# Optimization experiments

Hardware: AMD Instinct MI355X
Metric: run time of the kernel (lower is better)

Reference implementation:

```python
import jax, jax.numpy as jnp
import numpy as np
import math

B, LA, LB, D, H = 8, 2048, 2048, 512, 512

def setup_inputs() -> dict:
    key = jax.random.key(0)
    ks = jax.random.split(key, 6)
    return {
        "input_a": jax.random.normal(ks[0], (B, LA, D), dtype=jnp.float32),
        "input_b": jax.random.normal(ks[1], (B, LB, D), dtype=jnp.float32),
        "mask_a": jax.random.randint(ks[2], (B, LA), 0, 2, dtype=jnp.int32),
        "mask_b": jax.random.randint(ks[3], (B, LB), 0, 2, dtype=jnp.int32),
        "Wa": jax.random.normal(ks[4], (D, H), dtype=jnp.float32) * (1.0 / math.sqrt(D)),
        "ba": jnp.zeros((H,), dtype=jnp.float32),
        "Wb": jax.random.normal(ks[5], (D, H), dtype=jnp.float32) * (1.0 / math.sqrt(D)),
        "bb": jnp.zeros((H,), dtype=jnp.float32),
    }

def reference(input_a, input_b, mask_a, mask_b, Wa, ba, Wb, bb):
    scale = 1.0 / math.sqrt(D)  # math.sqrt(input_dim_a)
    mapped_a = input_a @ Wa + ba            # [B, La, H]
    mapped_b = input_b @ Wb + bb            # [B, Lb, H]
    # final_mask = (mask_a outer mask_b) == 0
    final_mask = (mask_a[:, :, None] * mask_b[:, None, :]) == 0  # [B, La, Lb]
    scores = jnp.einsum('bih,bjh->bij', mapped_a, mapped_b) * scale
    scores = jnp.where(final_mask, jnp.float32(-1e9), scores)
    # attentions_a = softmax over Lb; attentions_b^T = softmax over La axis
    att_a = jax.nn.softmax(scores, axis=-1)   # [B, La, Lb]
    att_bT = jax.nn.softmax(scores, axis=1)   # [B, La, Lb] (= attentions_b.transpose(1,2))
    output_a = jnp.einsum('bij,bjd->bid', att_bT, input_b)  # [B, La, D]
    output_b = jnp.einsum('bij,bid->bjd', att_a, input_a)   # [B, Lb, D]
    return (output_a + input_a, output_b + input_b)
```

## Files before the change

kernel.cpp:

```cpp
#include <hip/hip_runtime.h>
#include <hip/hip_bf16.h>

#define BATCH 8
#define LSEQ 2048
#define DDIM 512

using f32x4 = __attribute__((ext_vector_type(4))) float;
using s16x8 = __attribute__((ext_vector_type(8))) short;
using s16x4 = __attribute__((ext_vector_type(4))) short;

static __device__ __forceinline__ unsigned short f2b(float f) {
  __hip_bfloat16 h = __float2bfloat16(f);
  return __builtin_bit_cast(unsigned short, h);
}
static __device__ __forceinline__ float b2f(unsigned short u) {
  unsigned int v = ((unsigned int)u) << 16;
  return __builtin_bit_cast(float, v);
}

static __device__ __forceinline__ void gld16(const unsigned short* g, unsigned short* l) {
  __builtin_amdgcn_global_load_lds(
      (__attribute__((address_space(1))) void*)(g),
      (__attribute__((address_space(3))) void*)(l), 16, 0, 0);
}

__device__ __forceinline__ void mfma_kloop2(
    const unsigned short* __restrict__ A, const unsigned short* __restrict__ Bt,
    int K, int lda, int ldb, unsigned short* sA, unsigned short* sB,
    int tid, f32x4 acc[4][4]) {
  const int wave = tid >> 6, lane = tid & 63;
  const int wm = (wave >> 1) * 64, wn = (wave & 1) * 64;
  const int lr = lane & 15, lq = lane >> 4;
  const int srow = tid >> 2;
  const int sk = (tid & 3) * 8;
  unsigned short* dA0 = sA + wave * 512;
  unsigned short* dA1 = sA + 2048 + wave * 512;
  unsigned short* dB0 = sB + wave * 512;
  unsigned short* dB1 = sB + 2048 + wave * 512;
  const unsigned short* pa0 = A + (size_t)srow * lda + sk;
  const unsigned short* pa1 = A + (size_t)(srow + 64) * lda + sk;
  const unsigned short* pb0 = Bt + (size_t)srow * ldb + sk;
  const unsigned short* pb1 = Bt + (size_t)(srow + 64) * ldb + sk;
  gld16(pa0, dA0);
  gld16(pa1, dA1);
  gld16(pb0, dB0);
  gld16(pb1, dB1);
  asm volatile("s_waitcnt vmcnt(0)\ns_barrier" ::: "memory");
  int cur = 0;
  for (int k0 = 0; k0 < K; k0 += 32) {
    const int nxt = cur ^ 1;
    if (k0 + 32 < K) {
      const int off = nxt * 4096;
      gld16(pa0 + k0 + 32, dA0 + off);
      gld16(pa1 + k0 + 32, dA1 + off);
      gld16(pb0 + k0 + 32, dB0 + off);
      gld16(pb1 + k0 + 32, dB1 + off);
    }
    const unsigned short* cA = sA + cur * 4096;
    const unsigned short* cB = sB + cur * 4096;
    s16x8 af[4], bf[4];
#pragma unroll
    for (int r = 0; r < 4; ++r)
      af[r] = *(const s16x8*)(cA + (wm + r * 16 + lr) * 32 + lq * 8);
#pragma unroll
    for (int c = 0; c < 4; ++c)
      bf[c] = *(const s16x8*)(cB + (wn + c * 16 + lr) * 32 + lq * 8);
#pragma unroll
    for (int r = 0; r < 4; ++r)
#pragma unroll
      for (int c = 0; c < 4; ++c)
        acc[r][c] = __builtin_amdgcn_mfma_f32_16x16x32_bf16(af[r], bf[c], acc[r][c], 0, 0, 0);
    asm volatile("s_waitcnt vmcnt(0)\ns_barrier" ::: "memory");
    cur = nxt;
  }
}

__global__ __launch_bounds__(256) void k_prep(const float* __restrict__ in_a,
                                              const float* __restrict__ in_b,
                                              const int* __restrict__ ma,
                                              const int* __restrict__ mb,
                                              unsigned short* __restrict__ oa,
                                              unsigned short* __restrict__ ob,
                                              float* __restrict__ Pa,
                                              float* __restrict__ Pb) {
  int z = blockIdx.z;
  const float* in = z ? in_b : in_a;
  const int* mask = z ? mb : ma;
  unsigned short* o16 = z ? ob : oa;
  float* partial = z ? Pb : Pa;
  int b = blockIdx.y;
  int l0 = blockIdx.x * 32;
  __shared__ int sm[32];
  if (threadIdx.x < 32) sm[threadIdx.x] = mask[b * LSEQ + l0 + threadIdx.x];
  __syncthreads();
  int d = threadIdx.x * 2;
  const float* base = in + ((size_t)b * LSEQ + l0) * DDIM + d;
  unsigned short* obase = o16 + ((size_t)b * LSEQ + l0) * DDIM + d;
  float ax = 0.f, ay = 0.f;
#pragma unroll 4
  for (int r = 0; r < 32; ++r) {
    float2 v = *(const float2*)(base + (size_t)r * DDIM);
    ushort2 u; u.x = f2b(v.x); u.y = f2b(v.y);
    *(ushort2*)(obase + (size_t)r * DDIM) = u;
    if (sm[r] == 0) { ax += v.x; ay += v.y; }
  }
  float2 o; o.x = ax; o.y = ay;
  *(float2*)(partial + ((size_t)(b * 64 + blockIdx.x)) * DDIM + d) = o;
}

__global__ __launch_bounds__(256) void k_p2(const float* __restrict__ Pa,
                                            const float* __restrict__ Pb,
                                            float* __restrict__ Ca,
                                            float* __restrict__ Cb) {
  int g = blockIdx.x;
  const float* src = (g < 8) ? Pa : Pb;
  float* dst = (g < 8) ? Ca : Cb;
  int b = g & 7;
  int d = threadIdx.x * 2;
  float ax = 0.f, ay = 0.f;
  for (int c = 0; c < 64; ++c) {
    float2 v = *(const float2*)(src + ((size_t)(b * 64 + c)) * DDIM + d);
    ax += v.x; ay += v.y;
  }
  dst[b * DDIM + d] = ax * (1.0f / LSEQ);
  dst[b * DDIM + d + 1] = ay * (1.0f / LSEQ);
}

__global__ __launch_bounds__(256) void k_transposeW(const float* __restrict__ Wa,
                                                    const float* __restrict__ Wb,
                                                    unsigned short* __restrict__ WaT,
                                                    unsigned short* __restrict__ WbT) {
  int gidx = blockIdx.x * 256 + threadIdx.x;
  const float* W = (gidx < 512 * 512) ? Wa : Wb;
  unsigned short* WT = (gidx < 512 * 512) ? WaT : WbT;
  int idx = gidx & (512 * 512 - 1);
  int h = idx >> 9, d = idx & 511;
  WT[idx] = f2b(W[d * DDIM + h]);
}

__global__ __launch_bounds__(256) void k_gemm_bias(const unsigned short* __restrict__ a16,
                                                   const unsigned short* __restrict__ b16,
                                                   const unsigned short* __restrict__ WaT,
                                                   const unsigned short* __restrict__ WbT,
                                                   const float* __restrict__ ba,
                                                   const float* __restrict__ bb,
                                                   unsigned short* __restrict__ mapa,
                                                   unsigned short* __restrict__ mapb) {
  int id = blockIdx.x;
  int g = id >> 5, rem = id & 31;
  int bn = (rem >> 3) * 128;
  int f = g * 8 + (rem & 7);
  int bm = (f & 127) * 128;
  int z = f >> 7;
  const unsigned short* A = z ? b16 : a16;
  const unsigned short* Bt = z ? WbT : WaT;
  const float* bias = z ? bb : ba;
  unsigned short* Cout = z ? mapb : mapa;
  __shared__ __align__(16) unsigned short sA[2 * 128 * 32], sB[2 * 128 * 32];
  f32x4 acc[4][4];
  f32x4 zero = {0.f, 0.f, 0.f, 0.f};
#pragma unroll
  for (int r = 0; r < 4; ++r)
#pragma unroll
    for (int c = 0; c < 4; ++c) acc[r][c] = zero;
  mfma_kloop2(A + (size_t)bm * DDIM, Bt + (size_t)bn * DDIM, DDIM, DDIM, DDIM,
              sA, sB, threadIdx.x, acc);
  int wave = threadIdx.x >> 6, lane = threadIdx.x & 63;
  int wm = (wave >> 1) * 64, wn = (wave & 1) * 64, lr = lane & 15, lq = lane >> 4;
#pragma unroll
  for (int r = 0; r < 4; ++r)
#pragma unroll
    for (int c = 0; c < 4; ++c)
#pragma unroll
      for (int rr = 0; rr < 4; ++rr) {
        int row = bm + wm + r * 16 + lq * 4 + rr;
        int col = bn + wn + c * 16 + lr;
        Cout[(size_t)row * DDIM + col] = f2b(acc[r][c][rr] + bias[col]);
      }
}

__global__ __launch_bounds__(256) void k_scores(const unsigned short* __restrict__ mapa,
                                                const unsigned short* __restrict__ mapb,
                                                const int* __restrict__ mask_a,
                                                const int* __restrict__ mask_b,
                                                unsigned short* __restrict__ E,
                                                unsigned short* __restrict__ Et,
                                                float* __restrict__ Zrow,
                                                float* __restrict__ Zcol) {
  int id = blockIdx.x;
  int low = id & 7, rest = id >> 3;
  int sub = rest & 15, Ghi = rest >> 4;
  int G = Ghi * 8 + low;
  int b = G >> 4, super = G & 15;
  int bi = (((super >> 2) << 2) + (sub >> 2)) * 128;
  int bj = (((super & 3) << 2) + (sub & 3)) * 128;
  __shared__ __align__(16) unsigned short sA[2 * 128 * 32], sB[2 * 128 * 32];
  __shared__ int sMa[128], sMb[128];
  int tid = threadIdx.x;
  if (tid < 128)
    sMa[tid] = mask_a[b * LSEQ + bi + tid];
  else
    sMb[tid - 128] = mask_b[b * LSEQ + bj + tid - 128];
  __syncthreads();
  f32x4 acc[4][4];
  f32x4 zero = {0.f, 0.f, 0.f, 0.f};
#pragma unroll
  for (int r = 0; r < 4; ++r)
#pragma unroll
    for (int c = 0; c < 4; ++c) acc[r][c] = zero;
  mfma_kloop2(mapa + ((size_t)b * LSEQ + bi) * DDIM, mapb + ((size_t)b * LSEQ + bj) * DDIM,
              DDIM, DDIM, DDIM, sA, sB, tid, acc);
  const float scale = 0.044194173824159216f;
  int wave = tid >> 6, lane = tid & 63;
  int wm = (wave >> 1) * 64, wn = (wave & 1) * 64, lr = lane & 15, lq = lane >> 4;
  unsigned short* Eb = E + (size_t)b * LSEQ * LSEQ + (size_t)bi * LSEQ + bj;
  float colp[4] = {0.f, 0.f, 0.f, 0.f};
  float rowp[4][4];
  s16x4 ev4[4][4];
#pragma unroll
  for (int r = 0; r < 4; ++r) {
#pragma unroll
    for (int rr = 0; rr < 4; ++rr) rowp[r][rr] = 0.f;
#pragma unroll
    for (int c = 0; c < 4; ++c) {
      int jl = wn + c * 16 + lr;
      int mb_ = sMb[jl];
#pragma unroll
      for (int rr = 0; rr < 4; ++rr) {
        int il = wm + r * 16 + lq * 4 + rr;
        float e = (sMa[il] && mb_) ? __expf(acc[r][c][rr] * scale) : 0.f;
        rowp[r][rr] += e;
        colp[c] += e;
        unsigned short eb = f2b(e);
        ev4[r][c][rr] = (short)eb;
        Eb[(size_t)il * LSEQ + jl] = eb;
      }
    }
  }
#pragma unroll
  for (int r = 0; r < 4; ++r)
#pragma unroll
    for (int rr = 0; rr < 4; ++rr) {
      float v = rowp[r][rr];
      v += __shfl_xor(v, 1);
      v += __shfl_xor(v, 2);
      v += __shfl_xor(v, 4);
      v += __shfl_xor(v, 8);
      if (lr == 0) {
        int il = wm + r * 16 + lq * 4 + rr;
        atomicAdd(&Zrow[b * LSEQ + bi + il], v);
      }
    }
#pragma unroll
  for (int c = 0; c < 4; ++c) {
    float v = colp[c];
    v += __shfl_xor(v, 16);
    v += __shfl_xor(v, 32);
    if (lq == 0) atomicAdd(&Zcol[b * LSEQ + bj + wn + c * 16 + lr], v);
  }
  unsigned short* buf = sA;
  unsigned short* EtB = Et + (size_t)b * LSEQ * LSEQ + (size_t)bj * LSEQ + bi;
#pragma unroll
  for (int half = 0; half < 2; ++half) {
    __syncthreads();
    if ((wn != 0) == (half != 0)) {
#pragma unroll
      for (int r = 0; r < 4; ++r)
#pragma unroll
        for (int c = 0; c < 4; ++c) {
          int jl = c * 16 + lr;
          int il0 = wm + r * 16 + lq * 4;
          *(s16x4*)(buf + jl * 128 + (il0 ^ ((jl & 7) << 4))) = ev4[r][c];
        }
    }
    __syncthreads();
#pragma unroll
    for (int p = 0; p < 4; ++p) {
      int idx = p * 256 + tid;
      int jlr = idx >> 4, chk = idx & 15;
      s16x8 v = *(const s16x8*)(buf + jlr * 128 + ((chk * 8) ^ ((jlr & 7) << 4)));
      *(s16x8*)(EtB + (size_t)(half * 64 + jlr) * LSEQ + chk * 8) = v;
    }
  }
}

__global__ __launch_bounds__(256) void k_scaleT(const unsigned short* __restrict__ a16,
                                                const unsigned short* __restrict__ b16,
                                                const float* __restrict__ Zrow,
                                                const float* __restrict__ Zcol,
                                                unsigned short* __restrict__ atS,
                                                unsigned short* __restrict__ btS) {
  int zz = blockIdx.z;
  int b = zz & 7, sel = zz >> 3;
  const unsigned short* in = sel ? b16 : a16;
  const float* Z = sel ? Zcol : Zrow;
  unsigned short* out = sel ? btS : atS;
  int i0 = blockIdx.y * 64, d0 = blockIdx.x * 64;
  __shared__ unsigned short lt[64 * 65];
  __shared__ float zinv[64];
  if (threadIdx.x < 64) {
    float z = Z[b * LSEQ + i0 + threadIdx.x];
    zinv[threadIdx.x] = (z > 0.f) ? 1.f / z : 0.f;
  }
  __syncthreads();
  const unsigned short* ib = in + ((size_t)b * LSEQ + i0) * DDIM + d0;
#pragma unroll
  for (int p = 0; p < 16; ++p) {
    int idx = p * 256 + threadIdx.x;
    int dl = idx & 63, il = idx >> 6;
    lt[dl * 65 + il] = f2b(b2f(ib[(size_t)il * DDIM + dl]) * zinv[il]);
  }
  __syncthreads();
  unsigned short* ob = out + ((size_t)b * DDIM + d0) * LSEQ + i0;
#pragma unroll
  for (int p = 0; p < 16; ++p) {
    int idx = p * 256 + threadIdx.x;
    int il = idx & 63, dl = idx >> 6;
    ob[(size_t)dl * LSEQ + il] = lt[dl * 65 + il];
  }
}

__global__ __launch_bounds__(512, 2) void k_gemm_outs(
    const unsigned short* __restrict__ E, const unsigned short* __restrict__ Et,
    const unsigned short* __restrict__ btS, const unsigned short* __restrict__ atS,
    const unsigned short* __restrict__ a16, const unsigned short* __restrict__ b16,
    const float* __restrict__ Ca, const float* __restrict__ Cb,
    float* __restrict__ OutA, float* __restrict__ OutB) {
  int w = (blockIdx.x & 7) * 32 + (blockIdx.x >> 3);
  int mode = w >> 7;
  int r0 = w & 127;
  int b = r0 >> 4, tile = r0 & 15;
  int bm = (tile >> 1) * 256, bn = (tile & 1) * 256;
  const unsigned short* Aop = (mode ? Et : E) + (size_t)b * LSEQ * LSEQ + (size_t)bm * LSEQ;
  const unsigned short* Bop = (mode ? atS : btS) + (size_t)b * DDIM * LSEQ + (size_t)bn * LSEQ;
  const unsigned short* addin = mode ? b16 : a16;
  const float* Cvec = mode ? Ca : Cb;
  float* Out = mode ? OutB : OutA;

  __shared__ __align__(16) unsigned short sA[4 * 8192], sB[4 * 8192];
  const int tid = threadIdx.x;
  const int wave = tid >> 6, lane = tid & 63;
  const int wr = wave >> 2, wc = wave & 3;
  const int lr = lane & 15, lq = lane >> 4;

  const int srow = tid >> 2;
  const int kcsw = ((tid & 3) ^ (srow & 3)) * 8;
  const unsigned short* pa0 = Aop + (size_t)srow * LSEQ + kcsw;
  const unsigned short* pa1 = pa0 + (size_t)128 * LSEQ;
  const unsigned short* pb0 = Bop + (size_t)srow * LSEQ + kcsw;
  const unsigned short* pb1 = pb0 + (size_t)128 * LSEQ;
  unsigned short* dA = sA + wave * 512;
  unsigned short* dB = sB + wave * 512;

  int aoff[8], boff[4];
#pragma unroll
  for (int m = 0; m < 8; ++m)
    aoff[m] = (wr * 128 + m * 16 + lr) * 32 + (lq ^ (lr & 3)) * 8;
#pragma unroll
  for (int n = 0; n < 4; ++n)
    boff[n] = (wc * 64 + n * 16 + lr) * 32 + (lq ^ (lr & 3)) * 8;

  f32x4 acc[8][4];
  f32x4 zero = {0.f, 0.f, 0.f, 0.f};
#pragma unroll
  for (int m = 0; m < 8; ++m)
#pragma unroll
    for (int n = 0; n < 4; ++n) acc[m][n] = zero;

#define SGA(c) { const int sl_ = ((c) & 3) * 8192; \
  gld16(pa0 + (size_t)(c) * 32, dA + sl_); \
  gld16(pa1 + (size_t)(c) * 32, dA + sl_ + 4096); }
#define SGB(c) { const int sl_ = ((c) & 3) * 8192; \
  gld16(pb0 + (size_t)(c) * 32, dB + sl_); \
  gld16(pb1 + (size_t)(c) * 32, dB + sl_ + 4096); }

  SGA(0); SGB(0); SGA(1); SGB(1); SGA(2); SGB(2);
  asm volatile("s_waitcnt vmcnt(8)\ns_barrier" ::: "memory");

  for (int j = 0; j < 64; ++j) {
    const int sl = (j & 3) * 8192;
    s16x8 af[8];
#pragma unroll
    for (int m = 0; m < 8; ++m) af[m] = *(const s16x8*)(sA + sl + aoff[m]);
    s16x8 bf0 = *(const s16x8*)(sB + sl + boff[0]);
    s16x8 bf1 = *(const s16x8*)(sB + sl + boff[1]);
    if (j < 61) SGA(j + 3);
    __builtin_amdgcn_s_setprio(1);
#pragma unroll
    for (int m = 0; m < 8; ++m) {
      acc[m][0] = __builtin_amdgcn_mfma_f32_16x16x32_bf16(af[m], bf0, acc[m][0], 0, 0, 0);
      acc[m][1] = __builtin_amdgcn_mfma_f32_16x16x32_bf16(af[m], bf1, acc[m][1], 0, 0, 0);
    }
    __builtin_amdgcn_s_setprio(0);
    asm volatile("s_barrier" ::: "memory");
    s16x8 bf2 = *(const s16x8*)(sB + sl + boff[2]);
    s16x8 bf3 = *(const s16x8*)(sB + sl + boff[3]);
    if (j < 61) SGB(j + 3);
    __builtin_amdgcn_s_setprio(1);
#pragma unroll
    for (int m = 0; m < 8; ++m) {
      acc[m][2] = __builtin_amdgcn_mfma_f32_16x16x32_bf16(af[m], bf2, acc[m][2], 0, 0, 0);
      acc[m][3] = __builtin_amdgcn_mfma_f32_16x16x32_bf16(af[m], bf3, acc[m][3], 0, 0, 0);
    }
    __builtin_amdgcn_s_setprio(0);
    if (j < 61)
      asm volatile("s_waitcnt vmcnt(8)\ns_barrier" ::: "memory");
    else if (j == 61)
      asm volatile("s_waitcnt vmcnt(4)\ns_barrier" ::: "memory");
    else
      asm volatile("s_waitcnt vmcnt(0)\ns_barrier" ::: "memory");
  }
#undef SGA
#undef SGB

#pragma unroll
  for (int m = 0; m < 8; ++m)
#pragma unroll
    for (int n = 0; n < 4; ++n)
#pragma unroll
      for (int rr = 0; rr < 4; ++rr) {
        int row = bm + wr * 128 + m * 16 + lq * 4 + rr;
        int col = bn + wc * 64 + n * 16 + lr;
        size_t o = ((size_t)b * LSEQ + row) * DDIM + col;
        Out[o] = acc[m][n][rr] + b2f(addin[o]) + Cvec[b * DDIM + col];
      }
}

extern "C" void kernel_launch(void* const* d_in, const int* in_sizes, int n_in,
                              void* d_out, int out_size, void* d_ws, size_t ws_size,
                              hipStream_t stream) {
  (void)in_sizes; (void)n_in; (void)out_size; (void)ws_size;
  const float* in_a = (const float*)d_in[0];
  const float* in_b = (const float*)d_in[1];
  const int* ma = (const int*)d_in[2];
  const int* mb = (const int*)d_in[3];
  const float* Wa = (const float*)d_in[4];
  const float* ba = (const float*)d_in[5];
  const float* Wb = (const float*)d_in[6];
  const float* bb = (const float*)d_in[7];
  float* out = (float*)d_out;

  char* ws = (char*)d_ws;
  const size_t MB = 1ull << 20;
  unsigned short* a16 = (unsigned short*)(ws + 0 * MB);
  unsigned short* b16 = (unsigned short*)(ws + 16 * MB);
  unsigned short* WaT = (unsigned short*)(ws + 32 * MB);
  unsigned short* WbT = (unsigned short*)(ws + 32 * MB + 512 * 1024);
  unsigned short* mapa = (unsigned short*)(ws + 33 * MB);
  unsigned short* mapb = (unsigned short*)(ws + 49 * MB);
  unsigned short* E = (unsigned short*)(ws + 65 * MB);
  unsigned short* atS = (unsigned short*)(ws + 129 * MB);
  unsigned short* btS = (unsigned short*)(ws + 145 * MB);
  float* Zrow = (float*)(ws + 161 * MB);
  float* Zcol = (float*)(ws + 161 * MB + 65536);
  float* Ca = (float*)(ws + 161 * MB + 2 * 65536);
  float* Cb = (float*)(ws + 161 * MB + 2 * 65536 + 16384);
  float* Pa = (float*)(ws + 162 * MB);
  float* Pb = (float*)(ws + 163 * MB);
  unsigned short* Et = (unsigned short*)(ws + 164 * MB);

  hipMemsetAsync(Zrow, 0, 2 * 65536, stream);
  k_prep<<<dim3(64, 8, 2), 256, 0, stream>>>(in_a, in_b, ma, mb, a16, b16, Pa, Pb);
  k_transposeW<<<2048, 256, 0, stream>>>(Wa, Wb, WaT, WbT);
  k_p2<<<16, 256, 0, stream>>>(Pa, Pb, Ca, Cb);
  k_gemm_bias<<<1024, 256, 0, stream>>>(a16, b16, WaT, WbT, ba, bb, mapa, mapb);
  k_scores<<<2048, 256, 0, stream>>>(mapa, mapb, ma, mb, E, Et, Zrow, Zcol);
  k_scaleT<<<dim3(8, 32, 16), 256, 0, stream>>>(a16, b16, Zrow, Zcol, atS, btS);
  k_gemm_outs<<<256, 512, 0, stream>>>(E, Et, btS, atS, a16, b16, Ca, Cb,
                                       out, out + (size_t)BATCH * LSEQ * DDIM);
}
```

Before: 380.5 us.

## Drop double-buffered k-loop and transpose score tile in one LDS pass

Replaces the double-buffered global_load_lds k-loop with a single-buffer loop that loads, syncs, computes and syncs on every 32-wide k step. This halves LDS use in the projection GEMM. In the scores kernel, exponentiated bf16 values are now written straight into one full 128x128 swizzled LDS tile during the epilogue. The tile is then stored transposed in a single pass, instead of two half passes from a register array. The aim is lower register and LDS pressure and fewer barriers, at the cost of no longer overlapping global loads with MFMA work.

```diff
diff --git a/kernel.cpp b/kernel.cpp
--- a/kernel.cpp
+++ b/kernel.cpp
@@ -24,7 +24,7 @@
       (__attribute__((address_space(3))) void*)(l), 16, 0, 0);
 }
 
-__device__ __forceinline__ void mfma_kloop2(
+__device__ __forceinline__ void mfma_kloop(
     const unsigned short* __restrict__ A, const unsigned short* __restrict__ Bt,
     int K, int lda, int ldb, unsigned short* sA, unsigned short* sB,
     int tid, f32x4 acc[4][4]) {
@@ -41,37 +41,25 @@
   const unsigned short* pa1 = A + (size_t)(srow + 64) * lda + sk;
   const unsigned short* pb0 = Bt + (size_t)srow * ldb + sk;
   const unsigned short* pb1 = Bt + (size_t)(srow + 64) * ldb + sk;
-  gld16(pa0, dA0);
-  gld16(pa1, dA1);
-  gld16(pb0, dB0);
-  gld16(pb1, dB1);
-  asm volatile("s_waitcnt vmcnt(0)\ns_barrier" ::: "memory");
-  int cur = 0;
   for (int k0 = 0; k0 < K; k0 += 32) {
-    const int nxt = cur ^ 1;
-    if (k0 + 32 < K) {
-      const int off = nxt * 4096;
-      gld16(pa0 + k0 + 32, dA0 + off);
-      gld16(pa1 + k0 + 32, dA1 + off);
-      gld16(pb0 + k0 + 32, dB0 + off);
-      gld16(pb1 + k0 + 32, dB1 + off);
-    }
-    const unsigned short* cA = sA + cur * 4096;
-    const unsigned short* cB = sB + cur * 4096;
+    gld16(pa0 + k0, dA0);
+    gld16(pa1 + k0, dA1);
+    gld16(pb0 + k0, dB0);
+    gld16(pb1 + k0, dB1);
+    __syncthreads();
     s16x8 af[4], bf[4];
 #pragma unroll
     for (int r = 0; r < 4; ++r)
-      af[r] = *(const s16x8*)(cA + (wm + r * 16 + lr) * 32 + lq * 8);
+      af[r] = *(const s16x8*)(sA + (wm + r * 16 + lr) * 32 + lq * 8);
 #pragma unroll
     for (int c = 0; c < 4; ++c)
-      bf[c] = *(const s16x8*)(cB + (wn + c * 16 + lr) * 32 + lq * 8);
+      bf[c] = *(const s16x8*)(sB + (wn + c * 16 + lr) * 32 + lq * 8);
 #pragma unroll
     for (int r = 0; r < 4; ++r)
 #pragma unroll
       for (int c = 0; c < 4; ++c)
         acc[r][c] = __builtin_amdgcn_mfma_f32_16x16x32_bf16(af[r], bf[c], acc[r][c], 0, 0, 0);
-    asm volatile("s_waitcnt vmcnt(0)\ns_barrier" ::: "memory");
-    cur = nxt;
+    __syncthreads();
   }
 }
 
@@ -156,15 +144,15 @@
   const unsigned short* Bt = z ? WbT : WaT;
   const float* bias = z ? bb : ba;
   unsigned short* Cout = z ? mapb : mapa;
-  __shared__ __align__(16) unsigned short sA[2 * 128 * 32], sB[2 * 128 * 32];
+  __shared__ __align__(16) unsigned short sA[128 * 32], sB[128 * 32];
   f32x4 acc[4][4];
   f32x4 zero = {0.f, 0.f, 0.f, 0.f};
 #pragma unroll
   for (int r = 0; r < 4; ++r)
 #pragma unroll
     for (int c = 0; c < 4; ++c) acc[r][c] = zero;
-  mfma_kloop2(A + (size_t)bm * DDIM, Bt + (size_t)bn * DDIM, DDIM, DDIM, DDIM,
-              sA, sB, threadIdx.x, acc);
+  mfma_kloop(A + (size_t)bm * DDIM, Bt + (size_t)bn * DDIM, DDIM, DDIM, DDIM,
+             sA, sB, threadIdx.x, acc);
   int wave = threadIdx.x >> 6, lane = threadIdx.x & 63;
   int wm = (wave >> 1) * 64, wn = (wave & 1) * 64, lr = lane & 15, lq = lane >> 4;
 #pragma unroll
@@ -194,29 +182,27 @@
   int b = G >> 4, super = G & 15;
   int bi = (((super >> 2) << 2) + (sub >> 2)) * 128;
   int bj = (((super & 3) << 2) + (sub & 3)) * 128;
-  __shared__ __align__(16) unsigned short sA[2 * 128 * 32], sB[2 * 128 * 32];
+  __shared__ __align__(16) unsigned short smem[16384];
   __shared__ int sMa[128], sMb[128];
   int tid = threadIdx.x;
   if (tid < 128)
     sMa[tid] = mask_a[b * LSEQ + bi + tid];
   else
     sMb[tid - 128] = mask_b[b * LSEQ + bj + tid - 128];
-  __syncthreads();
   f32x4 acc[4][4];
   f32x4 zero = {0.f, 0.f, 0.f, 0.f};
 #pragma unroll
   for (int r = 0; r < 4; ++r)
 #pragma unroll
     for (int c = 0; c < 4; ++c) acc[r][c] = zero;
-  mfma_kloop2(mapa + ((size_t)b * LSEQ + bi) * DDIM, mapb + ((size_t)b * LSEQ + bj) * DDIM,
-              DDIM, DDIM, DDIM, sA, sB, tid, acc);
+  mfma_kloop(mapa + ((size_t)b * LSEQ + bi) * DDIM, mapb + ((size_t)b * LSEQ + bj) * DDIM,
+             DDIM, DDIM, DDIM, smem, smem + 4096, tid, acc);
   const float scale = 0.044194173824159216f;
   int wave = tid >> 6, lane = tid & 63;
   int wm = (wave >> 1) * 64, wn = (wave & 1) * 64, lr = lane & 15, lq = lane >> 4;
   unsigned short* Eb = E + (size_t)b * LSEQ * LSEQ + (size_t)bi * LSEQ + bj;
   float colp[4] = {0.f, 0.f, 0.f, 0.f};
   float rowp[4][4];
-  s16x4 ev4[4][4];
 #pragma unroll
   for (int r = 0; r < 4; ++r) {
 #pragma unroll
@@ -225,6 +211,7 @@
     for (int c = 0; c < 4; ++c) {
       int jl = wn + c * 16 + lr;
       int mb_ = sMb[jl];
+      s16x4 t;
 #pragma unroll
       for (int rr = 0; rr < 4; ++rr) {
         int il = wm + r * 16 + lq * 4 + rr;
@@ -232,9 +219,11 @@
         rowp[r][rr] += e;
         colp[c] += e;
         unsigned short eb = f2b(e);
-        ev4[r][c][rr] = (short)eb;
+        t[rr] = (short)eb;
         Eb[(size_t)il * LSEQ + jl] = eb;
       }
+      int il0 = wm + r * 16 + lq * 4;
+      *(s16x4*)(smem + jl * 128 + (il0 ^ ((jl & 7) << 4))) = t;
     }
   }
 #pragma unroll
@@ -258,29 +247,14 @@
     v += __shfl_xor(v, 32);
     if (lq == 0) atomicAdd(&Zcol[b * LSEQ + bj + wn + c * 16 + lr], v);
   }
-  unsigned short* buf = sA;
+  __syncthreads();
   unsigned short* EtB = Et + (size_t)b * LSEQ * LSEQ + (size_t)bj * LSEQ + bi;
 #pragma unroll
-  for (int half = 0; half < 2; ++half) {
-    __syncthreads();
-    if ((wn != 0) == (half != 0)) {
-#pragma unroll
-      for (int r = 0; r < 4; ++r)
-#pragma unroll
-        for (int c = 0; c < 4; ++c) {
-          int jl = c * 16 + lr;
-          int il0 = wm + r * 16 + lq * 4;
-          *(s16x4*)(buf + jl * 128 + (il0 ^ ((jl & 7) << 4))) = ev4[r][c];
-        }
-    }
-    __syncthreads();
-#pragma unroll
-    for (int p = 0; p < 4; ++p) {
-      int idx = p * 256 + tid;
-      int jlr = idx >> 4, chk = idx & 15;
-      s16x8 v = *(const s16x8*)(buf + jlr * 128 + ((chk * 8) ^ ((jlr & 7) << 4)));
-      *(s16x8*)(EtB + (size_t)(half * 64 + jlr) * LSEQ + chk * 8) = v;
-    }
+  for (int p = 0; p < 8; ++p) {
+    int idx = p * 256 + tid;
+    int jlr = idx >> 4, chk = idx & 15;
+    s16x8 v = *(const s16x8*)(smem + jlr * 128 + ((chk * 8) ^ ((jlr & 7) << 4)));
+    *(s16x8*)(EtB + (size_t)jlr * LSEQ + chk * 8) = v;
   }
 }
 
```

Result: faster. 324.7 us (-14.7%).
